# Kernel tuning notes

Hardware: AMD Instinct MI355X
Metric: run time of the kernel (lower is better)

Reference implementation:

```python
import jax, jax.numpy as jnp
import numpy as np

VERTEX_W = 1.0
SMOOTH_W = 0.1
SYM_W = 0.05
CHAMFER_W = 0.1

B, N = 4, 8192  # N points per cloud, flat dim = N*3


def setup_inputs() -> dict:
    key = jax.random.key(0)
    k1, k2 = jax.random.split(key)
    pred = jax.random.normal(k1, (B, N * 3), dtype=jnp.float32)
    targ = jax.random.normal(k2, (B, N * 3), dtype=jnp.float32)
    return {"pred_vertices": pred, "target_vertices": targ}


def _chamfer(x, y):
    # x: [B,N,3], y: [B,M,3]; euclidean cdist via matmul expansion
    x2 = jnp.sum(x * x, axis=-1)  # [B,N]
    y2 = jnp.sum(y * y, axis=-1)  # [B,M]
    xy = jnp.einsum('bnd,bmd->bnm', x, y)  # [B,N,M]
    d2 = x2[:, :, None] + y2[None if False else slice(None), None, :] - 2.0 * xy
    d = jnp.sqrt(jnp.maximum(d2, 0.0))
    return jnp.mean(jnp.min(d, axis=2)) + jnp.mean(jnp.min(d, axis=1))


def reference(pred_vertices, target_vertices):
    b = pred_vertices.shape[0]
    pv = pred_vertices.reshape(b, -1, 3)
    tv = target_vertices.reshape(b, -1, 3)

    # vertex MSE (on flat tensors, same as mse on reshaped)
    vertex_loss = jnp.mean((pred_vertices - target_vertices) ** 2)

    # smoothness: mean L2 norm of consecutive vertex diffs
    diff = pv[:, 1:, :] - pv[:, :-1, :]
    smoothness_loss = jnp.mean(jnp.linalg.norm(diff, axis=2))

    # symmetry: N is even in this config
    mid = pv.shape[1] // 2
    left = pv[:, :mid, :]
    right = jnp.flip(pv[:, mid:, :], axis=1)
    right = right.at[:, :, 0].multiply(-1.0)
    symmetry_loss = jnp.mean((left - right) ** 2)

    chamfer_loss = _chamfer(pv, tv)

    total = (VERTEX_W * vertex_loss + SMOOTH_W * smoothness_loss
             + SYM_W * symmetry_loss + CHAMFER_W * chamfer_loss)
    return total
```

## Files before the change

kernel.cpp:

```cpp
#include <hip/hip_runtime.h>
#include <hip/hip_bf16.h>


#define B_ 4
#define N_ 8192
#define MID_ (N_ / 2)
#define CNT_OFF 1536
#define RP_OFF 1664
#define PM_OFF 4096
#define PMC_OFF (PM_OFF + 8 * B_ * N_)

typedef short short8 __attribute__((ext_vector_type(8)));
typedef float f32x16 __attribute__((ext_vector_type(16)));

__global__ void AdvancedLoss3D_1881195675843_kernel() {}

__device__ inline unsigned short bfu(float x) {
    union { __hip_bfloat16 b; unsigned short u; } c;
    c.b = __float2bfloat16(x);
    return c.u;
}
__device__ inline float bff(unsigned short u) {
    union { __hip_bfloat16 b; unsigned short u; } c;
    c.u = u;
    return __bfloat162float(c.b);
}

__device__ __forceinline__ float min3f(float a, float b, float c) {
    return fminf(fminf(a, b), c);
}
__device__ __forceinline__ float tree16(f32x16 v) {
    float m0 = min3f(v[0],  v[1],  v[2]);
    float m1 = min3f(v[3],  v[4],  v[5]);
    float m2 = min3f(v[6],  v[7],  v[8]);
    float m3 = min3f(v[9],  v[10], v[11]);
    float m4 = min3f(v[12], v[13], v[14]);
    return fminf(min3f(m0, m1, m2), min3f(m3, m4, v[15]));
}

__device__ __forceinline__ short8 encA_half(float x, float y, float z, int kh) {
    float n2 = fmaf(x, x, fmaf(y, y, z * z));
    unsigned short hx = bfu(x), hy = bfu(y), hz = bfu(z);
    float fx = bff(hx), fy = bff(hy), fz = bff(hz);
    unsigned short lx = bfu(x - fx), ly = bfu(y - fy), lz = bfu(z - fz);
    unsigned short mx = bfu(-2.f * fx), my = bfu(-2.f * fy), mz = bfu(-2.f * fz);
    unsigned short nx = bfu(-2.f * bff(lx)), ny = bfu(-2.f * bff(ly)),
                   nz = bfu(-2.f * bff(lz));
    unsigned short n2h = bfu(n2);
    unsigned short n2l = bfu(n2 - bff(n2h));
    unsigned short one = bfu(1.0f);
    short8 lo = {(short)mx, (short)my, (short)mz, (short)mx,
                 (short)my, (short)mz, (short)nx, (short)ny};
    short8 hi = {(short)nz, (short)n2h, (short)n2l, (short)one,
                 (short)one, 0, 0, 0};
    return kh ? hi : lo;
}
__device__ __forceinline__ void encB(float x, float y, float z,
                                     unsigned short* Bv) {
    float n2 = fmaf(x, x, fmaf(y, y, z * z));
    unsigned short hx = bfu(x), hy = bfu(y), hz = bfu(z);
    float fx = bff(hx), fy = bff(hy), fz = bff(hz);
    unsigned short lx = bfu(x - fx), ly = bfu(y - fy), lz = bfu(z - fz);
    unsigned short n2h = bfu(n2);
    unsigned short n2l = bfu(n2 - bff(n2h));
    unsigned short one = bfu(1.0f);
    Bv[0] = hx; Bv[1] = hy; Bv[2] = hz;
    Bv[3] = lx; Bv[4] = ly; Bv[5] = lz;
    Bv[6] = hx; Bv[7] = hy; Bv[8] = hz;
    Bv[9] = one; Bv[10] = one; Bv[11] = n2h; Bv[12] = n2l;
    Bv[13] = Bv[14] = Bv[15] = 0;
}

__global__ __launch_bounds__(256, 2) void chamfer_mfma(const float* __restrict__ pred,
                                                       const float* __restrict__ targ,
                                                       float* __restrict__ ws) {
    int bid = blockIdx.x;
    int chunk = bid & 31;
    int rgb = bid >> 5;
    int b   = chunk >> 3;
    int cc  = chunk & 7;
    int tid = threadIdx.x;
    int w   = tid >> 6;
    int l   = tid & 63;
    int lr  = l & 31;
    int kh  = l >> 5;

    if (bid == 0 && tid == 0)
        ((unsigned int*)ws)[CNT_OFF] = 0u;

    __shared__ __align__(16) unsigned char smem[65536];
    float (*colbuf)[1024] = (float (*)[1024])(smem + 32768);

    {
        const float* tb = targ + (size_t)(b * N_ + cc * 1024) * 3;
#pragma unroll
        for (int j = 0; j < 4; j++) {
            int c = tid + 256 * j;
            float x = tb[3 * c], y = tb[3 * c + 1], z = tb[3 * c + 2];
            union { unsigned short s[16]; uint4 q[2]; } e;
            encB(x, y, z, e.s);
            unsigned char* base = smem + (size_t)(c >> 5) * 1024 + (c & 31) * 16;
            *(uint4*)(base)       = e.q[0];
            *(uint4*)(base + 512) = e.q[1];
        }
    }

    int rowbase = (rgb * 4 + w) * 128;
    short8 af[4];
    {
        const float* pb = pred + (size_t)(b * N_ + rowbase + lr) * 3;
#pragma unroll
        for (int i = 0; i < 4; i++)
            af[i] = encA_half(pb[i * 96], pb[i * 96 + 1], pb[i * 96 + 2], kh);
    }

    float rmin[4][16];
#pragma unroll
    for (int i = 0; i < 4; i++)
#pragma unroll
        for (int j = 0; j < 16; j++) rmin[i][j] = 3.4e38f;

    __syncthreads();

    const f32x16 zero = {0.f, 0.f, 0.f, 0.f, 0.f, 0.f, 0.f, 0.f,
                         0.f, 0.f, 0.f, 0.f, 0.f, 0.f, 0.f, 0.f};
    const unsigned char* bl = smem + kh * 512 + lr * 16;
    for (int t = 0; t < 32; t += 2) {
        short8 bE = *(const short8*)(bl + (size_t)t * 1024);
        short8 bO = *(const short8*)(bl + (size_t)(t + 1) * 1024);
        float cmE = 3.4e38f, cmO = 3.4e38f;
#pragma unroll
        for (int i = 0; i < 4; i++) {
            f32x16 aE = __builtin_amdgcn_mfma_f32_32x32x16_bf16(af[i], bE, zero, 0, 0, 0);
            f32x16 aO = __builtin_amdgcn_mfma_f32_32x32x16_bf16(af[i], bO, zero, 0, 0, 0);
#pragma unroll
            for (int j = 0; j < 16; j++)
                rmin[i][j] = min3f(rmin[i][j], aE[j], aO[j]);
            cmE = fminf(cmE, tree16(aE));
            cmO = fminf(cmO, tree16(aO));
        }
        cmE = fminf(cmE, __shfl_xor(cmE, 32, 64));
        cmO = fminf(cmO, __shfl_xor(cmO, 32, 64));
        colbuf[w][t * 32 + lr] = cmE;
        colbuf[w][(t + 1) * 32 + lr] = cmO;
    }
    __syncthreads();

    {
        float* pmc = ws + PMC_OFF + (size_t)rgb * 32768 + b * N_ + cc * 1024;
#pragma unroll
        for (int c0 = 0; c0 < 1024; c0 += 256) {
            int c = c0 + tid;
            pmc[c] = fminf(fminf(colbuf[0][c], colbuf[1][c]),
                           fminf(colbuf[2][c], colbuf[3][c]));
        }
    }
    __syncthreads();

    float (*sred)[128][32] = (float (*)[128][32])smem;
#pragma unroll
    for (int i = 0; i < 4; i++)
#pragma unroll
        for (int j = 0; j < 16; j++) {
            int r = i * 32 + (j & 3) + 8 * (j >> 2) + 4 * kh;
            sred[w][r][(lr + r) & 31] = rmin[i][j];
        }
    __syncthreads();
    float* orow = ws + PM_OFF + (size_t)cc * 32768 + b * N_ + rowbase;
#pragma unroll
    for (int rr = 0; rr < 128; rr += 64) {
        int r = rr + l;
        float v = 3.4e38f;
#pragma unroll
        for (int c = 0; c < 32; c++)
            v = fminf(v, sred[w][r][(c + r) & 31]);
        orow[r] = v;
    }
}

__global__ __launch_bounds__(256) void reduce_compose(const float* __restrict__ pred,
                                                      const float* __restrict__ targ,
                                                      float* __restrict__ ws,
                                                      unsigned int* __restrict__ out) {
    int bid = blockIdx.x, tid = threadIdx.x;
    int idx = bid * 256 + tid;
    float v = 3.4e38f;
    float dv = 0.f, sm = 0.f, sy = 0.f;
    if (idx < B_ * N_) {
        const float* pmr = ws + PM_OFF;
#pragma unroll
        for (int s = 0; s < 8; s++)
            v = fminf(v, pmr[(size_t)s * 32768 + idx]);

        int b = idx >> 13;
        int i = idx & (N_ - 1);
        const float* p = pred + (size_t)idx * 3;
        const float* t = targ + (size_t)idx * 3;
        float px = p[0], py = p[1], pz = p[2];
        float tx = t[0], ty = t[1], tz = t[2];
        float dx = px - tx, dy = py - ty, dz = pz - tz;
        dv = dx * dx + dy * dy + dz * dz;
        if (i < N_ - 1) {
            float ex = p[3] - px, ey = p[4] - py, ez = p[5] - pz;
            sm = sqrtf(ex * ex + ey * ey + ez * ez);
        }
        if (i < MID_) {
            const float* r = pred + ((size_t)(b * N_ + (N_ - 1 - i))) * 3;
            float ax = px + r[0];
            float ay = py - r[1];
            float az = pz - r[2];
            sy = ax * ax + ay * ay + az * az;
        }
    } else {
        int c = idx - B_ * N_;
        const float* pmc = ws + PMC_OFF;
#pragma unroll
        for (int s = 0; s < 16; s++)
            v = fminf(v, pmc[(size_t)s * 32768 + c]);
    }
    float d = sqrtf(fmaxf(v, 0.f));
    for (int off = 32; off; off >>= 1) {
        d  += __shfl_down(d, off, 64);
        dv += __shfl_down(dv, off, 64);
        sm += __shfl_down(sm, off, 64);
        sy += __shfl_down(sy, off, 64);
    }
    __shared__ float red[4][4];
    __shared__ int is_last;
    int lane = tid & 63, w = tid >> 6;
    if (lane == 0) { red[0][w] = d; red[1][w] = dv; red[2][w] = sm; red[3][w] = sy; }
    __syncthreads();
    if (tid == 0) {
        ws[RP_OFF + bid] = red[0][0] + red[0][1] + red[0][2] + red[0][3];
        ws[3 * bid + 0]  = red[1][0] + red[1][1] + red[1][2] + red[1][3];
        ws[3 * bid + 1]  = red[2][0] + red[2][1] + red[2][2] + red[2][3];
        ws[3 * bid + 2]  = red[3][0] + red[3][1] + red[3][2] + red[3][3];
        __threadfence();
        unsigned old = atomicAdd((unsigned int*)ws + CNT_OFF, 1u);
        is_last = (old == 255u);
    }
    __syncthreads();
    if (!is_last) return;

    if (tid == 0) __threadfence();
    __syncthreads();
    float rp = ws[RP_OFF + tid];
    float cr = (tid < 128) ? rp : 0.f;
    float cc = (tid < 128) ? 0.f : rp;
    float dvs = ws[3 * tid], sms = ws[3 * tid + 1], sys = ws[3 * tid + 2];
    for (int off = 32; off; off >>= 1) {
        dvs += __shfl_down(dvs, off, 64);
        sms += __shfl_down(sms, off, 64);
        sys += __shfl_down(sys, off, 64);
        cr  += __shfl_down(cr, off, 64);
        cc  += __shfl_down(cc, off, 64);
    }
    __shared__ float red5[5][4];
    if (lane == 0) { red5[0][w] = dvs; red5[1][w] = sms; red5[2][w] = sys;
                     red5[3][w] = cr;  red5[4][w] = cc; }
    __syncthreads();
    if (tid == 0) {
        float S[5];
#pragma unroll
        for (int q = 0; q < 5; q++)
            S[q] = red5[q][0] + red5[q][1] + red5[q][2] + red5[q][3];
        float vertex = S[0] / (float)(B_ * N_ * 3);
        float smooth = S[1] / (float)(B_ * (N_ - 1));
        float sym    = S[2] / (float)(B_ * MID_ * 3);
        float cham   = (S[3] + S[4]) / (float)(B_ * N_);
        float total  = vertex + 0.1f * smooth + 0.05f * sym + 0.1f * cham;
        union { __hip_bfloat16 b; unsigned short u; } cv;
        cv.b = __float2bfloat16(total);
        out[0] = ((unsigned int)cv.u << 16) | (unsigned int)cv.u;
    }
}

extern "C" void kernel_launch(void* const* d_in, const int* in_sizes, int n_in,
                              void* d_out, int out_size, void* d_ws, size_t ws_size,
                              hipStream_t stream) {
    (void)in_sizes; (void)n_in; (void)out_size; (void)ws_size;
    const float* pred = (const float*)d_in[0];
    const float* targ = (const float*)d_in[1];
    float* wsf = (float*)d_ws;

    chamfer_mfma<<<dim3(512), dim3(256), 0, stream>>>(pred, targ, wsf);
    reduce_compose<<<dim3(256), dim3(256), 0, stream>>>(
        pred, targ, wsf, (unsigned int*)d_out);
}
```

Measured before the change: 79.16 us.

## Fuse final reduction into chamfer kernel via per-group last-block atomics

Removes the second reduce kernel launch. The chamfer kernel now uses atomic counters per row group and per column group, so the last block to finish each group reduces its partial minima and computes the vertex, smoothness and symmetry terms. A global counter then lets the final block compose the total loss. The counters are zeroed with a memset on the stream, which adds an extra operation in place of the removed kernel launch.

Result: slower. 149.5 us (+88.8%).

```diff
diff --git a/kernel.cpp b/kernel.cpp
--- a/kernel.cpp
+++ b/kernel.cpp
@@ -5,8 +5,12 @@
 #define B_ 4
 #define N_ 8192
 #define MID_ (N_ / 2)
-#define CNT_OFF 1536
-#define RP_OFF 1664
+#define CTR_U 1536
+#define RS_OFF 1664
+#define DV_OFF 1728
+#define SM_OFF 1792
+#define SY_OFF 1856
+#define CS_OFF 1920
 #define PM_OFF 4096
 #define PMC_OFF (PM_OFF + 8 * B_ * N_)
 
@@ -71,9 +75,10 @@
     Bv[13] = Bv[14] = Bv[15] = 0;
 }
 
-__global__ __launch_bounds__(256, 2) void chamfer_mfma(const float* __restrict__ pred,
-                                                       const float* __restrict__ targ,
-                                                       float* __restrict__ ws) {
+__global__ __launch_bounds__(256, 2) void chamfer_all(const float* __restrict__ pred,
+                                                      const float* __restrict__ targ,
+                                                      float* __restrict__ ws,
+                                                      unsigned int* __restrict__ out) {
     int bid = blockIdx.x;
     int chunk = bid & 31;
     int rgb = bid >> 5;
@@ -85,11 +90,9 @@
     int lr  = l & 31;
     int kh  = l >> 5;
 
-    if (bid == 0 && tid == 0)
-        ((unsigned int*)ws)[CNT_OFF] = 0u;
-
     __shared__ __align__(16) unsigned char smem[65536];
     float (*colbuf)[1024] = (float (*)[1024])(smem + 32768);
+    unsigned int* ctr = (unsigned int*)ws + CTR_U;
 
     {
         const float* tb = targ + (size_t)(b * N_ + cc * 1024) * 3;
@@ -176,102 +179,121 @@
             v = fminf(v, sred[w][r][(c + r) & 31]);
         orow[r] = v;
     }
-}
-
-__global__ __launch_bounds__(256) void reduce_compose(const float* __restrict__ pred,
-                                                      const float* __restrict__ targ,
-                                                      float* __restrict__ ws,
-                                                      unsigned int* __restrict__ out) {
-    int bid = blockIdx.x, tid = threadIdx.x;
-    int idx = bid * 256 + tid;
-    float v = 3.4e38f;
-    float dv = 0.f, sm = 0.f, sy = 0.f;
-    if (idx < B_ * N_) {
+
+    __shared__ int rlast, clast, glast;
+    float (*red4)[4] = (float (*)[4])smem;
+    int lane = tid & 63;
+
+    __threadfence();
+    __syncthreads();
+
+    int rowg = b * 16 + rgb;
+    if (tid == 0) rlast = (atomicAdd(ctr + rowg, 1u) == 7u);
+    __syncthreads();
+    if (rlast) {
+        if (tid == 0) __threadfence();
+        __syncthreads();
+        float dsum = 0.f, dv = 0.f, smv = 0.f, syv = 0.f;
         const float* pmr = ws + PM_OFF;
 #pragma unroll
-        for (int s = 0; s < 8; s++)
-            v = fminf(v, pmr[(size_t)s * 32768 + idx]);
-
-        int b = idx >> 13;
-        int i = idx & (N_ - 1);
-        const float* p = pred + (size_t)idx * 3;
-        const float* t = targ + (size_t)idx * 3;
-        float px = p[0], py = p[1], pz = p[2];
-        float tx = t[0], ty = t[1], tz = t[2];
-        float dx = px - tx, dy = py - ty, dz = pz - tz;
-        dv = dx * dx + dy * dy + dz * dz;
-        if (i < N_ - 1) {
-            float ex = p[3] - px, ey = p[4] - py, ez = p[5] - pz;
-            sm = sqrtf(ex * ex + ey * ey + ez * ez);
-        }
-        if (i < MID_) {
-            const float* r = pred + ((size_t)(b * N_ + (N_ - 1 - i))) * 3;
-            float ax = px + r[0];
-            float ay = py - r[1];
-            float az = pz - r[2];
-            sy = ax * ax + ay * ay + az * az;
-        }
-    } else {
-        int c = idx - B_ * N_;
+        for (int k = 0; k < 2; k++) {
+            int r = rgb * 512 + tid + k * 256;
+            int idx = b * N_ + r;
+            float v = 3.4e38f;
+#pragma unroll
+            for (int s = 0; s < 8; s++)
+                v = fminf(v, pmr[(size_t)s * 32768 + idx]);
+            dsum += sqrtf(fmaxf(v, 0.f));
+            const float* p = pred + (size_t)idx * 3;
+            const float* t = targ + (size_t)idx * 3;
+            float px = p[0], py = p[1], pz = p[2];
+            float dx = px - t[0], dy = py - t[1], dz = pz - t[2];
+            dv += dx * dx + dy * dy + dz * dz;
+            if (r < N_ - 1) {
+                float ex = p[3] - px, ey = p[4] - py, ez = p[5] - pz;
+                smv += sqrtf(ex * ex + ey * ey + ez * ez);
+            }
+            if (r < MID_) {
+                const float* q = pred + ((size_t)(b * N_ + (N_ - 1 - r))) * 3;
+                float ax = px + q[0], ay = py - q[1], az = pz - q[2];
+                syv += ax * ax + ay * ay + az * az;
+            }
+        }
+        for (int off = 32; off; off >>= 1) {
+            dsum += __shfl_down(dsum, off, 64);
+            dv   += __shfl_down(dv, off, 64);
+            smv  += __shfl_down(smv, off, 64);
+            syv  += __shfl_down(syv, off, 64);
+        }
+        if (lane == 0) { red4[0][w] = dsum; red4[1][w] = dv;
+                         red4[2][w] = smv;  red4[3][w] = syv; }
+        __syncthreads();
+        if (tid == 0) {
+            ws[RS_OFF + rowg] = red4[0][0] + red4[0][1] + red4[0][2] + red4[0][3];
+            ws[DV_OFF + rowg] = red4[1][0] + red4[1][1] + red4[1][2] + red4[1][3];
+            ws[SM_OFF + rowg] = red4[2][0] + red4[2][1] + red4[2][2] + red4[2][3];
+            ws[SY_OFF + rowg] = red4[3][0] + red4[3][1] + red4[3][2] + red4[3][3];
+        }
+        __syncthreads();
+    }
+
+    int colg = b * 8 + cc;
+    if (tid == 0) clast = (atomicAdd(ctr + 64 + colg, 1u) == 15u);
+    __syncthreads();
+    if (clast) {
+        if (tid == 0) __threadfence();
+        __syncthreads();
+        float csum = 0.f;
         const float* pmc = ws + PMC_OFF;
 #pragma unroll
-        for (int s = 0; s < 16; s++)
-            v = fminf(v, pmc[(size_t)s * 32768 + c]);
-    }
-    float d = sqrtf(fmaxf(v, 0.f));
-    for (int off = 32; off; off >>= 1) {
-        d  += __shfl_down(d, off, 64);
-        dv += __shfl_down(dv, off, 64);
-        sm += __shfl_down(sm, off, 64);
-        sy += __shfl_down(sy, off, 64);
-    }
-    __shared__ float red[4][4];
-    __shared__ int is_last;
-    int lane = tid & 63, w = tid >> 6;
-    if (lane == 0) { red[0][w] = d; red[1][w] = dv; red[2][w] = sm; red[3][w] = sy; }
-    __syncthreads();
-    if (tid == 0) {
-        ws[RP_OFF + bid] = red[0][0] + red[0][1] + red[0][2] + red[0][3];
-        ws[3 * bid + 0]  = red[1][0] + red[1][1] + red[1][2] + red[1][3];
-        ws[3 * bid + 1]  = red[2][0] + red[2][1] + red[2][2] + red[2][3];
-        ws[3 * bid + 2]  = red[3][0] + red[3][1] + red[3][2] + red[3][3];
-        __threadfence();
-        unsigned old = atomicAdd((unsigned int*)ws + CNT_OFF, 1u);
-        is_last = (old == 255u);
-    }
-    __syncthreads();
-    if (!is_last) return;
-
+        for (int k = 0; k < 4; k++) {
+            int c = cc * 1024 + tid + k * 256;
+            int idx = b * N_ + c;
+            float v = 3.4e38f;
+#pragma unroll
+            for (int s = 0; s < 16; s++)
+                v = fminf(v, pmc[(size_t)s * 32768 + idx]);
+            csum += sqrtf(fmaxf(v, 0.f));
+        }
+        for (int off = 32; off; off >>= 1) csum += __shfl_down(csum, off, 64);
+        if (lane == 0) red4[0][w] = csum;
+        __syncthreads();
+        if (tid == 0)
+            ws[CS_OFF + colg] = red4[0][0] + red4[0][1] + red4[0][2] + red4[0][3];
+        __syncthreads();
+    }
+
+    __threadfence();
+    __syncthreads();
+    if (tid == 0) glast = (atomicAdd(ctr + 96, 1u) == 511u);
+    __syncthreads();
+    if (!glast) return;
     if (tid == 0) __threadfence();
     __syncthreads();
-    float rp = ws[RP_OFF + tid];
-    float cr = (tid < 128) ? rp : 0.f;
-    float cc = (tid < 128) ? 0.f : rp;
-    float dvs = ws[3 * tid], sms = ws[3 * tid + 1], sys = ws[3 * tid + 2];
-    for (int off = 32; off; off >>= 1) {
-        dvs += __shfl_down(dvs, off, 64);
-        sms += __shfl_down(sms, off, 64);
-        sys += __shfl_down(sys, off, 64);
-        cr  += __shfl_down(cr, off, 64);
-        cc  += __shfl_down(cc, off, 64);
-    }
-    __shared__ float red5[5][4];
-    if (lane == 0) { red5[0][w] = dvs; red5[1][w] = sms; red5[2][w] = sys;
-                     red5[3][w] = cr;  red5[4][w] = cc; }
-    __syncthreads();
-    if (tid == 0) {
-        float S[5];
-#pragma unroll
-        for (int q = 0; q < 5; q++)
-            S[q] = red5[q][0] + red5[q][1] + red5[q][2] + red5[q][3];
-        float vertex = S[0] / (float)(B_ * N_ * 3);
-        float smooth = S[1] / (float)(B_ * (N_ - 1));
-        float sym    = S[2] / (float)(B_ * MID_ * 3);
-        float cham   = (S[3] + S[4]) / (float)(B_ * N_);
-        float total  = vertex + 0.1f * smooth + 0.05f * sym + 0.1f * cham;
-        union { __hip_bfloat16 b; unsigned short u; } cv;
-        cv.b = __float2bfloat16(total);
-        out[0] = ((unsigned int)cv.u << 16) | (unsigned int)cv.u;
+
+    if (tid < 64) {
+        float rs  = ws[RS_OFF + tid];
+        float dvv = ws[DV_OFF + tid];
+        float smv = ws[SM_OFF + tid];
+        float syv = ws[SY_OFF + tid];
+        float cs  = (tid < 32) ? ws[CS_OFF + tid] : 0.f;
+        for (int off = 32; off; off >>= 1) {
+            rs  += __shfl_down(rs, off, 64);
+            dvv += __shfl_down(dvv, off, 64);
+            smv += __shfl_down(smv, off, 64);
+            syv += __shfl_down(syv, off, 64);
+            cs  += __shfl_down(cs, off, 64);
+        }
+        if (tid == 0) {
+            float vertex = dvv / (float)(B_ * N_ * 3);
+            float smooth = smv / (float)(B_ * (N_ - 1));
+            float sym    = syv / (float)(B_ * MID_ * 3);
+            float cham   = (rs + cs) / (float)(B_ * N_);
+            float total  = vertex + 0.1f * smooth + 0.05f * sym + 0.1f * cham;
+            union { __hip_bfloat16 b; unsigned short u; } cv;
+            cv.b = __float2bfloat16(total);
+            out[0] = ((unsigned int)cv.u << 16) | (unsigned int)cv.u;
+        }
     }
 }
 
@@ -283,7 +305,7 @@
     const float* targ = (const float*)d_in[1];
     float* wsf = (float*)d_ws;
 
-    chamfer_mfma<<<dim3(512), dim3(256), 0, stream>>>(pred, targ, wsf);
-    reduce_compose<<<dim3(256), dim3(256), 0, stream>>>(
-        pred, targ, wsf, (unsigned int*)d_out);
-}
+    hipMemsetAsync((char*)d_ws + (size_t)CTR_U * 4, 0, 512, stream);
+    chamfer_all<<<dim3(512), dim3(256), 0, stream>>>(pred, targ, wsf,
+                                                     (unsigned int*)d_out);
+}
```
